# Kernel optimization log

Measured on AMD Instinct MI355X. Metric: run time of the kernel, lower is better.

The kernel has to match this reference:

```python
import jax, jax.numpy as jnp
import numpy as np

ALPHA = 0.2  # leaky relu negative slope (LinearNet default)


def _init_linear(key, fan_in, fan_out):
    kw, kb = jax.random.split(key)
    lim = 1.0 / np.sqrt(fan_in)
    W = jax.random.uniform(kw, (fan_in, fan_out), jnp.float32, -lim, lim)
    b = jax.random.uniform(kb, (fan_out,), jnp.float32, -lim, lim)
    return W, b


def setup_inputs() -> dict:
    key = jax.random.key(0)
    keys = jax.random.split(key, 8)
    B, N, F = 8, 512, 32
    x = jax.random.normal(keys[0], (B, N, F), jnp.float32)
    # fe: [2F=64 -> 64 -> 64 -> 64], all layers leaky-relu (final_linear=False)
    fe_W0, fe_b0 = _init_linear(keys[1], 2 * F, 64)
    fe_W1, fe_b1 = _init_linear(keys[2], 64, 64)
    fe_W2, fe_b2 = _init_linear(keys[3], 64, 64)
    # fn: [64 + F = 96 -> 128 -> 128 -> 32], last layer linear (final_linear=True)
    fn_W0, fn_b0 = _init_linear(keys[4], 64 + F, 128)
    fn_W1, fn_b1 = _init_linear(keys[5], 128, 128)
    fn_W2, fn_b2 = _init_linear(keys[6], 128, 32)
    return {
        "x": x,
        "fe_W0": fe_W0, "fe_b0": fe_b0,
        "fe_W1": fe_W1, "fe_b1": fe_b1,
        "fe_W2": fe_W2, "fe_b2": fe_b2,
        "fn_W0": fn_W0, "fn_b0": fn_b0,
        "fn_W1": fn_W1, "fn_b1": fn_b1,
        "fn_W2": fn_W2, "fn_b2": fn_b2,
    }


def reference(x, fe_W0, fe_b0, fe_W1, fe_b1, fe_W2, fe_b2,
              fn_W0, fn_b0, fn_W1, fn_b1, fn_W2, fn_b2):
    B, N, F = x.shape
    # all-pairs edge inputs: A[b,i,j] = concat(x[b,i], x[b,j])  (x1=repeat rows, x2=tile)
    xi = jnp.broadcast_to(x[:, :, None, :], (B, N, N, F))
    xj = jnp.broadcast_to(x[:, None, :, :], (B, N, N, F))
    A = jnp.concatenate([xi, xj], axis=-1)  # [B, N, N, 2F]
    # edge MLP fe: leaky relu after every layer (final_linear=False)
    for W, b in ((fe_W0, fe_b0), (fe_W1, fe_b1), (fe_W2, fe_b2)):
        A = jax.nn.leaky_relu(A @ W + b, negative_slope=ALPHA)
    # sum aggregation over the sender axis j
    agg = jnp.sum(A, axis=2)  # [B, N, K]
    h = jnp.concatenate([agg, x], axis=-1)  # [B, N, K + F]
    # node MLP fn: leaky relu on hidden layers, final layer linear
    h = jax.nn.leaky_relu(h @ fn_W0 + fn_b0, negative_slope=ALPHA)
    h = jax.nn.leaky_relu(h @ fn_W1 + fn_b1, negative_slope=ALPHA)
    out = h @ fn_W2 + fn_b2  # [B, N, output_node_size]
    return out
```

## Files before the change

kernel.cpp:

```cpp
#include <hip/hip_runtime.h>
#include <hip/hip_bf16.h>

#define ALPHA 0.2f
static __device__ __forceinline__ float lrel(float x) { return fmaxf(x, ALPHA * x); }

typedef __attribute__((ext_vector_type(8))) short bf16x8;
typedef __attribute__((ext_vector_type(4))) float f32x4;

union FragU { bf16x8 v; unsigned int u[4]; uint4 q; };

static __device__ __forceinline__ unsigned int pk2(float a, float b) {
    unsigned int r;
    asm("v_cvt_pk_bf16_f32 %0, %1, %2" : "=v"(r) : "v"(a), "v"(b));
    return r;
}
static __device__ __forceinline__ unsigned int cvl2(float a, float b) {
    return pk2(lrel(a), lrel(b));
}
static __device__ __forceinline__ unsigned short f2bf(float x) {
    union { float f; unsigned int u; } c;
    c.f = x;
    unsigned int r = c.u + 0x7FFFu + ((c.u >> 16) & 1u);
    return (unsigned short)(r >> 16);
}
static __device__ __forceinline__ int pi64(int s) {
    return 32 * ((s >> 4) >> 1) + 8 * ((s >> 2) & 3) + 4 * ((s >> 4) & 1) + (s & 3);
}

__global__ __launch_bounds__(256) void k_uv(
    const float* __restrict__ x, const float* __restrict__ W0, const float* __restrict__ b0,
    const float* __restrict__ W1, const float* __restrict__ W2,
    float* __restrict__ Upi, unsigned short* __restrict__ xbf, unsigned int* __restrict__ WF)
{
    if (blockIdx.x == 1024) {
        const int t = threadIdx.x;
        const int l = t & 63, part = t >> 6;
        const int lo = l & 15, g = l >> 4;
        for (int ff = part; ff < 20; ff += 4) {
            unsigned int o[4];
            if (ff < 4) {
                const int nf = ff;
                const int pc = 32 * (nf >> 1) + 8 * (lo >> 2) + 4 * (nf & 1) + (lo & 3);
#pragma unroll
                for (int uq = 0; uq < 4; ++uq) {
                    const int k0 = 8 * g + 2 * uq;
                    o[uq] = pk2(W0[(32 + k0) * 64 + pc], W0[(33 + k0) * 64 + pc]);
                }
            } else if (ff < 12) {
                const int s = (ff - 4) >> 2, nf = (ff - 4) & 3;
                const int pc = 32 * (nf >> 1) + 8 * (lo >> 2) + 4 * (nf & 1) + (lo & 3);
#pragma unroll
                for (int uq = 0; uq < 4; ++uq) {
                    const int k0 = 32 * s + 8 * g + 2 * uq;
                    o[uq] = pk2(W1[k0 * 64 + pc], W1[(k0 + 1) * 64 + pc]);
                }
            } else {
                const int s = (ff - 12) >> 2, nf = (ff - 12) & 3;
                const int c2 = 16 * nf + lo;
#pragma unroll
                for (int uq = 0; uq < 4; ++uq) {
                    const int k0 = 32 * s + 8 * g + 2 * uq;
                    o[uq] = pk2(W2[k0 * 64 + c2], W2[(k0 + 1) * 64 + c2]);
                }
            }
            *(uint4*)(WF + (ff * 64 + l) * 4) = make_uint4(o[0], o[1], o[2], o[3]);
        }
        return;
    }
    const int idx = blockIdx.x * 256 + threadIdx.x;
    const int n = idx >> 6;
    const int slot = idx & 63;
    const int f = pi64(slot);
    const float* xr = x + n * 32;
    float u = b0[f];
#pragma unroll
    for (int i = 0; i < 32; ++i) u += xr[i] * W0[i * 64 + f];
    Upi[idx] = u;
    if (slot < 32) xbf[n * 32 + slot] = f2bf(xr[slot]);
}

__global__ __launch_bounds__(256, 3) void k_edge(
    const float* __restrict__ Upi, const unsigned short* __restrict__ xbf,
    const unsigned int* __restrict__ WF,
    const float* __restrict__ b1, const float* __restrict__ b2,
    float* __restrict__ AGG)
{
    __shared__ uint4 wlds[1024];
    const int tid = threadIdx.x;
    const int w = tid >> 6, l = tid & 63;
    const int lo = l & 15, g = l >> 4;
    const int bid = blockIdx.x;
    const int b = bid >> 7, ig = bid & 127;
    const int node = b * 512 + ig * 4 + w;

    for (int idx = tid; idx < 1024; idx += 256)
        wlds[idx] = ((const uint4*)WF)[256 + idx];

    FragU w0f[4];
    const uint4* wp = (const uint4*)WF;
#pragma unroll
    for (int nf = 0; nf < 4; ++nf) w0f[nf].q = wp[nf * 64 + l];

    f32x4 u0f[4], b1f[4], b2f[4];
#pragma unroll
    for (int nf = 0; nf < 4; ++nf) {
        const float4 t0 = *(const float4*)(Upi + node * 64 + nf * 16 + 4 * g);
        u0f[nf] = (f32x4){t0.x, t0.y, t0.z, t0.w};
        const float4 t1 = *(const float4*)(b1 + 32 * (nf >> 1) + 8 * g + 4 * (nf & 1));
        const float4 t2 = *(const float4*)(b2 + 16 * nf + 4 * g);
        b1f[nf] = (f32x4){t1.x, t1.y, t1.z, t1.w};
        b2f[nf] = (f32x4){t2.x, t2.y, t2.z, t2.w};
    }

    const unsigned short* xb = xbf + b * 512 * 32;
    FragU xj;
    xj.q = *(const uint4*)(xb + lo * 32 + 8 * g);

    f32x4 agg[4];
#pragma unroll
    for (int nf = 0; nf < 4; ++nf) { f32x4 z = {0.f, 0.f, 0.f, 0.f}; agg[nf] = z; }

    __syncthreads();

#pragma unroll 1
    for (int k = 0; k < 32; ++k) {
        int widx = 0;
        asm volatile("" : "+v"(widx));

        const int jn = ((k + 1) & 31) * 16;
        FragU xjn;
        xjn.q = *(const uint4*)(xb + (jn + lo) * 32 + 8 * g);

        f32x4 acc0[4];
#pragma unroll
        for (int nf = 0; nf < 4; ++nf)
            acc0[nf] = __builtin_amdgcn_mfma_f32_16x16x32_bf16(w0f[nf].v, xj.v, u0f[nf], 0, 0, 0);

        FragU q0, q1;
        q0.u[0] = cvl2(acc0[0][0], acc0[0][1]);
        q0.u[1] = cvl2(acc0[0][2], acc0[0][3]);
        q0.u[2] = cvl2(acc0[1][0], acc0[1][1]);
        q0.u[3] = cvl2(acc0[1][2], acc0[1][3]);
        q1.u[0] = cvl2(acc0[2][0], acc0[2][1]);
        q1.u[1] = cvl2(acc0[2][2], acc0[2][3]);
        q1.u[2] = cvl2(acc0[3][0], acc0[3][1]);
        q1.u[3] = cvl2(acc0[3][2], acc0[3][3]);

        f32x4 acc1[4];
#pragma unroll
        for (int nf = 0; nf < 4; ++nf) {
            FragU wa, wb;
            wa.q = wlds[widx + nf * 64 + l];
            wb.q = wlds[widx + (4 + nf) * 64 + l];
            acc1[nf] = __builtin_amdgcn_mfma_f32_16x16x32_bf16(wa.v, q0.v, b1f[nf], 0, 0, 0);
            acc1[nf] = __builtin_amdgcn_mfma_f32_16x16x32_bf16(wb.v, q1.v, acc1[nf], 0, 0, 0);
        }

        FragU p0, p1;
        p0.u[0] = cvl2(acc1[0][0], acc1[0][1]);
        p0.u[1] = cvl2(acc1[0][2], acc1[0][3]);
        p0.u[2] = cvl2(acc1[1][0], acc1[1][1]);
        p0.u[3] = cvl2(acc1[1][2], acc1[1][3]);
        p1.u[0] = cvl2(acc1[2][0], acc1[2][1]);
        p1.u[1] = cvl2(acc1[2][2], acc1[2][3]);
        p1.u[2] = cvl2(acc1[3][0], acc1[3][1]);
        p1.u[3] = cvl2(acc1[3][2], acc1[3][3]);

        f32x4 acc2[4];
#pragma unroll
        for (int nf = 0; nf < 4; ++nf) {
            FragU wa, wb;
            wa.q = wlds[widx + (8 + nf) * 64 + l];
            wb.q = wlds[widx + (12 + nf) * 64 + l];
            acc2[nf] = __builtin_amdgcn_mfma_f32_16x16x32_bf16(wa.v, p0.v, b2f[nf], 0, 0, 0);
            acc2[nf] = __builtin_amdgcn_mfma_f32_16x16x32_bf16(wb.v, p1.v, acc2[nf], 0, 0, 0);
        }

#pragma unroll
        for (int nf = 0; nf < 4; ++nf)
#pragma unroll
            for (int r = 0; r < 4; ++r) agg[nf][r] += lrel(acc2[nf][r]);

        xj = xjn;
    }

#pragma unroll
    for (int nf = 0; nf < 4; ++nf)
#pragma unroll
        for (int r = 0; r < 4; ++r) {
            float v = agg[nf][r];
            v += __shfl_xor(v, 1);
            v += __shfl_xor(v, 2);
            v += __shfl_xor(v, 4);
            v += __shfl_xor(v, 8);
            agg[nf][r] = v;
        }
    if (lo == 0) {
#pragma unroll
        for (int nf = 0; nf < 4; ++nf) {
            float4 o = {agg[nf][0], agg[nf][1], agg[nf][2], agg[nf][3]};
            *(float4*)(AGG + node * 64 + 16 * nf + 4 * g) = o;
        }
    }
}

__global__ __launch_bounds__(256) void k_fn(
    const float* __restrict__ AGG, const float* __restrict__ x,
    const float* __restrict__ W0, const float* __restrict__ b0,
    const float* __restrict__ W1, const float* __restrict__ b1,
    const float* __restrict__ W2, const float* __restrict__ b2,
    float* __restrict__ out)
{
    __shared__ float in96T[96][8];
    __shared__ float h1T[128][8];
    __shared__ float h2T[128][8];
    const int t = threadIdx.x;
    const int half = t >> 7, f = t & 127;
    const int node0 = blockIdx.x * 8;

    for (int idx = t; idx < 768; idx += 256) {
        int nn = idx & 7, k = idx >> 3;
        in96T[k][nn] = (k < 64) ? AGG[(node0 + nn) * 64 + k]
                                : x[(node0 + nn) * 32 + (k - 64)];
    }
    __syncthreads();

    {
        float a0 = b0[f], a1 = a0, a2 = a0, a3 = a0;
#pragma unroll 4
        for (int k = 0; k < 96; ++k) {
            const float4 iv = *(const float4*)(&in96T[k][4 * half]);
            const float wv = W0[k * 128 + f];
            a0 += iv.x * wv; a1 += iv.y * wv; a2 += iv.z * wv; a3 += iv.w * wv;
        }
        float4 o = {lrel(a0), lrel(a1), lrel(a2), lrel(a3)};
        *(float4*)(&h1T[f][4 * half]) = o;
    }
    __syncthreads();

    {
        float a0 = b1[f], a1 = a0, a2 = a0, a3 = a0;
#pragma unroll 4
        for (int k = 0; k < 128; ++k) {
            const float4 iv = *(const float4*)(&h1T[k][4 * half]);
            const float wv = W1[k * 128 + f];
            a0 += iv.x * wv; a1 += iv.y * wv; a2 += iv.z * wv; a3 += iv.w * wv;
        }
        float4 o = {lrel(a0), lrel(a1), lrel(a2), lrel(a3)};
        *(float4*)(&h2T[f][4 * half]) = o;
    }
    __syncthreads();

    {
        const int nn = t >> 5, fo = t & 31;
        float a = b2[fo];
#pragma unroll 4
        for (int k = 0; k < 128; ++k) a += h2T[k][nn] * W2[k * 32 + fo];
        out[(node0 + nn) * 32 + fo] = a;
    }
}

extern "C" void kernel_launch(void* const* d_in, const int* in_sizes, int n_in,
                              void* d_out, int out_size, void* d_ws, size_t ws_size,
                              hipStream_t stream)
{
    const float* x    = (const float*)d_in[0];
    const float* feW0 = (const float*)d_in[1];
    const float* feb0 = (const float*)d_in[2];
    const float* feW1 = (const float*)d_in[3];
    const float* feb1 = (const float*)d_in[4];
    const float* feW2 = (const float*)d_in[5];
    const float* feb2 = (const float*)d_in[6];
    const float* fnW0 = (const float*)d_in[7];
    const float* fnb0 = (const float*)d_in[8];
    const float* fnW1 = (const float*)d_in[9];
    const float* fnb1 = (const float*)d_in[10];
    const float* fnW2 = (const float*)d_in[11];
    const float* fnb2 = (const float*)d_in[12];
    float* out = (float*)d_out;

    float* Upi = (float*)d_ws;
    float* AGG = Upi + 262144;
    unsigned short* xbf = (unsigned short*)(AGG + 262144);
    unsigned int* WF = (unsigned int*)(xbf + 131072);

    hipLaunchKernelGGL(k_uv,   dim3(1025), dim3(256), 0, stream, x, feW0, feb0, feW1, feW2, Upi, xbf, WF);
    hipLaunchKernelGGL(k_edge, dim3(1024), dim3(256), 0, stream, Upi, xbf, WF, feb1, feb2, AGG);
    hipLaunchKernelGGL(k_fn,   dim3(512),  dim3(256), 0, stream, AGG, x, fnW0, fnb0, fnW1, fnb1, fnW2, fnb2, out);
}
```

Measured before the change: 83.14 us.

## Software-pipeline edge MLP layers across iterations and split leaky-relu sum algebraically

The edge loop is software-pipelined. Layer-0 MFMAs for the next j-tile are issued while the current tile goes through layer 1, and the layer-2 output is accumulated one iteration late, overlapping MFMA latency with VALU conversion work. The leaky-relu-then-sum is rewritten as 0.6*sum(x)+0.4*sum(|x|), using a VALU add with the abs source modifier, and x is prefetched two tiles ahead. Occupancy hint drops from 3 to 2 blocks per CU to make room for the extra live registers, at the risk of less latency hiding across waves.

Result: faster. 74.54 us (-10.3%).

```diff
diff --git a/kernel.cpp b/kernel.cpp
--- a/kernel.cpp
+++ b/kernel.cpp
@@ -16,6 +16,9 @@
 }
 static __device__ __forceinline__ unsigned int cvl2(float a, float b) {
     return pk2(lrel(a), lrel(b));
+}
+static __device__ __forceinline__ void addabs(float& a, float x) {
+    asm("v_add_f32 %0, %0, |%1|" : "+v"(a) : "v"(x));
 }
 static __device__ __forceinline__ unsigned short f2bf(float x) {
     union { float f; unsigned int u; } c;
@@ -79,7 +82,7 @@
     if (slot < 32) xbf[n * 32 + slot] = f2bf(xr[slot]);
 }
 
-__global__ __launch_bounds__(256, 3) void k_edge(
+__global__ __launch_bounds__(256, 2) void k_edge(
     const float* __restrict__ Upi, const unsigned short* __restrict__ xbf,
     const unsigned int* __restrict__ WF,
     const float* __restrict__ b1, const float* __restrict__ b2,
@@ -113,38 +116,52 @@
     }
 
     const unsigned short* xb = xbf + b * 512 * 32;
-    FragU xj;
-    xj.q = *(const uint4*)(xb + lo * 32 + 8 * g);
-
-    f32x4 agg[4];
-#pragma unroll
-    for (int nf = 0; nf < 4; ++nf) { f32x4 z = {0.f, 0.f, 0.f, 0.f}; agg[nf] = z; }
+
+    FragU xjB, xjN;
+    xjB.q = *(const uint4*)(xb + lo * 32 + 8 * g);
+    xjN.q = *(const uint4*)(xb + (16 + lo) * 32 + 8 * g);
 
     __syncthreads();
 
-#pragma unroll 1
+    f32x4 acc0c[4];
+#pragma unroll
+    for (int nf = 0; nf < 4; ++nf)
+        acc0c[nf] = __builtin_amdgcn_mfma_f32_16x16x32_bf16(w0f[nf].v, xjB.v, u0f[nf], 0, 0, 0);
+    xjB = xjN;
+
+    f32x4 acc2p[4];
+#pragma unroll
+    for (int nf = 0; nf < 4; ++nf) { f32x4 z = {0.f, 0.f, 0.f, 0.f}; acc2p[nf] = z; }
+
+    float aggL[4][4], aggA[4][4];
+#pragma unroll
+    for (int nf = 0; nf < 4; ++nf)
+#pragma unroll
+        for (int r = 0; r < 4; ++r) { aggL[nf][r] = 0.f; aggA[nf][r] = 0.f; }
+
+#pragma unroll 2
     for (int k = 0; k < 32; ++k) {
         int widx = 0;
         asm volatile("" : "+v"(widx));
 
-        const int jn = ((k + 1) & 31) * 16;
+        const int jn = ((k + 2) & 31) * 16;
         FragU xjn;
         xjn.q = *(const uint4*)(xb + (jn + lo) * 32 + 8 * g);
 
-        f32x4 acc0[4];
+        f32x4 acc0n[4];
 #pragma unroll
         for (int nf = 0; nf < 4; ++nf)
-            acc0[nf] = __builtin_amdgcn_mfma_f32_16x16x32_bf16(w0f[nf].v, xj.v, u0f[nf], 0, 0, 0);
+            acc0n[nf] = __builtin_amdgcn_mfma_f32_16x16x32_bf16(w0f[nf].v, xjB.v, u0f[nf], 0, 0, 0);
 
         FragU q0, q1;
-        q0.u[0] = cvl2(acc0[0][0], acc0[0][1]);
-        q0.u[1] = cvl2(acc0[0][2], acc0[0][3]);
-        q0.u[2] = cvl2(acc0[1][0], acc0[1][1]);
-        q0.u[3] = cvl2(acc0[1][2], acc0[1][3]);
-        q1.u[0] = cvl2(acc0[2][0], acc0[2][1]);
-        q1.u[1] = cvl2(acc0[2][2], acc0[2][3]);
-        q1.u[2] = cvl2(acc0[3][0], acc0[3][1]);
-        q1.u[3] = cvl2(acc0[3][2], acc0[3][3]);
+        q0.u[0] = cvl2(acc0c[0][0], acc0c[0][1]);
+        q0.u[1] = cvl2(acc0c[0][2], acc0c[0][3]);
+        q0.u[2] = cvl2(acc0c[1][0], acc0c[1][1]);
+        q0.u[3] = cvl2(acc0c[1][2], acc0c[1][3]);
+        q1.u[0] = cvl2(acc0c[2][0], acc0c[2][1]);
+        q1.u[1] = cvl2(acc0c[2][2], acc0c[2][3]);
+        q1.u[2] = cvl2(acc0c[3][0], acc0c[3][1]);
+        q1.u[3] = cvl2(acc0c[3][2], acc0c[3][3]);
 
         f32x4 acc1[4];
 #pragma unroll
@@ -155,6 +172,14 @@
             acc1[nf] = __builtin_amdgcn_mfma_f32_16x16x32_bf16(wa.v, q0.v, b1f[nf], 0, 0, 0);
             acc1[nf] = __builtin_amdgcn_mfma_f32_16x16x32_bf16(wb.v, q1.v, acc1[nf], 0, 0, 0);
         }
+
+#pragma unroll
+        for (int nf = 0; nf < 4; ++nf)
+#pragma unroll
+            for (int r = 0; r < 4; ++r) {
+                aggL[nf][r] += acc2p[nf][r];
+                addabs(aggA[nf][r], acc2p[nf][r]);
+            }
 
         FragU p0, p1;
         p0.u[0] = cvl2(acc1[0][0], acc1[0][1]);
@@ -166,39 +191,43 @@
         p1.u[2] = cvl2(acc1[3][0], acc1[3][1]);
         p1.u[3] = cvl2(acc1[3][2], acc1[3][3]);
 
-        f32x4 acc2[4];
 #pragma unroll
         for (int nf = 0; nf < 4; ++nf) {
             FragU wa, wb;
             wa.q = wlds[widx + (8 + nf) * 64 + l];
             wb.q = wlds[widx + (12 + nf) * 64 + l];
-            acc2[nf] = __builtin_amdgcn_mfma_f32_16x16x32_bf16(wa.v, p0.v, b2f[nf], 0, 0, 0);
-            acc2[nf] = __builtin_amdgcn_mfma_f32_16x16x32_bf16(wb.v, p1.v, acc2[nf], 0, 0, 0);
-        }
-
-#pragma unroll
-        for (int nf = 0; nf < 4; ++nf)
-#pragma unroll
-            for (int r = 0; r < 4; ++r) agg[nf][r] += lrel(acc2[nf][r]);
-
-        xj = xjn;
+            acc2p[nf] = __builtin_amdgcn_mfma_f32_16x16x32_bf16(wa.v, p0.v, b2f[nf], 0, 0, 0);
+            acc2p[nf] = __builtin_amdgcn_mfma_f32_16x16x32_bf16(wb.v, p1.v, acc2p[nf], 0, 0, 0);
+        }
+
+#pragma unroll
+        for (int nf = 0; nf < 4; ++nf) acc0c[nf] = acc0n[nf];
+        xjB = xjn;
     }
 
 #pragma unroll
     for (int nf = 0; nf < 4; ++nf)
 #pragma unroll
         for (int r = 0; r < 4; ++r) {
-            float v = agg[nf][r];
+            aggL[nf][r] += acc2p[nf][r];
+            addabs(aggA[nf][r], acc2p[nf][r]);
+        }
+
+#pragma unroll
+    for (int nf = 0; nf < 4; ++nf)
+#pragma unroll
+        for (int r = 0; r < 4; ++r) {
+            float v = 0.6f * aggL[nf][r] + 0.4f * aggA[nf][r];
             v += __shfl_xor(v, 1);
             v += __shfl_xor(v, 2);
             v += __shfl_xor(v, 4);
             v += __shfl_xor(v, 8);
-            agg[nf][r] = v;
+            aggL[nf][r] = v;
         }
     if (lo == 0) {
 #pragma unroll
         for (int nf = 0; nf < 4; ++nf) {
-            float4 o = {agg[nf][0], agg[nf][1], agg[nf][2], agg[nf][3]};
+            float4 o = {aggL[nf][0], aggL[nf][1], aggL[nf][2], aggL[nf][3]};
             *(float4*)(AGG + node * 64 + 16 * nf + 4 * g) = o;
         }
     }
```

## Process two receiver nodes per wave in edge kernel to reuse weights

Applied to the files above, without the earlier changes.

Each wave in the edge MLP kernel now handles two receiver nodes instead of one. The two nodes share the x_j fragments and the weight fragments read from LDS, and their independent MFMA chains are interleaved to hide latency. The grid is halved to 512 blocks and the occupancy hint drops from 3 to 2 blocks per SM to make room for the doubled accumulator registers. The trade-off is fewer resident waves, and 512 blocks may not fill all compute units evenly.

Result: faster. 77.31 us (-7.0%).

```diff
diff --git a/kernel.cpp b/kernel.cpp
--- a/kernel.cpp
+++ b/kernel.cpp
@@ -79,7 +79,7 @@
     if (slot < 32) xbf[n * 32 + slot] = f2bf(xr[slot]);
 }
 
-__global__ __launch_bounds__(256, 3) void k_edge(
+__global__ __launch_bounds__(256, 2) void k_edge(
     const float* __restrict__ Upi, const unsigned short* __restrict__ xbf,
     const unsigned int* __restrict__ WF,
     const float* __restrict__ b1, const float* __restrict__ b2,
@@ -90,8 +90,9 @@
     const int w = tid >> 6, l = tid & 63;
     const int lo = l & 15, g = l >> 4;
     const int bid = blockIdx.x;
-    const int b = bid >> 7, ig = bid & 127;
-    const int node = b * 512 + ig * 4 + w;
+    const int b = bid >> 6, ig = bid & 63;
+    const int nodeA = b * 512 + ig * 8 + w;
+    const int nodeB = nodeA + 4;
 
     for (int idx = tid; idx < 1024; idx += 256)
         wlds[idx] = ((const uint4*)WF)[256 + idx];
@@ -101,11 +102,13 @@
 #pragma unroll
     for (int nf = 0; nf < 4; ++nf) w0f[nf].q = wp[nf * 64 + l];
 
-    f32x4 u0f[4], b1f[4], b2f[4];
+    f32x4 uA[4], uB[4], b1f[4], b2f[4];
 #pragma unroll
     for (int nf = 0; nf < 4; ++nf) {
-        const float4 t0 = *(const float4*)(Upi + node * 64 + nf * 16 + 4 * g);
-        u0f[nf] = (f32x4){t0.x, t0.y, t0.z, t0.w};
+        const float4 ta = *(const float4*)(Upi + nodeA * 64 + nf * 16 + 4 * g);
+        const float4 tb = *(const float4*)(Upi + nodeB * 64 + nf * 16 + 4 * g);
+        uA[nf] = (f32x4){ta.x, ta.y, ta.z, ta.w};
+        uB[nf] = (f32x4){tb.x, tb.y, tb.z, tb.w};
         const float4 t1 = *(const float4*)(b1 + 32 * (nf >> 1) + 8 * g + 4 * (nf & 1));
         const float4 t2 = *(const float4*)(b2 + 16 * nf + 4 * g);
         b1f[nf] = (f32x4){t1.x, t1.y, t1.z, t1.w};
@@ -116,9 +119,11 @@
     FragU xj;
     xj.q = *(const uint4*)(xb + lo * 32 + 8 * g);
 
-    f32x4 agg[4];
-#pragma unroll
-    for (int nf = 0; nf < 4; ++nf) { f32x4 z = {0.f, 0.f, 0.f, 0.f}; agg[nf] = z; }
+    float aggA[4][4], aggB[4][4];
+#pragma unroll
+    for (int nf = 0; nf < 4; ++nf)
+#pragma unroll
+        for (int r = 0; r < 4; ++r) { aggA[nf][r] = 0.f; aggB[nf][r] = 0.f; }
 
     __syncthreads();
 
@@ -131,55 +136,101 @@
         FragU xjn;
         xjn.q = *(const uint4*)(xb + (jn + lo) * 32 + 8 * g);
 
-        f32x4 acc0[4];
-#pragma unroll
-        for (int nf = 0; nf < 4; ++nf)
-            acc0[nf] = __builtin_amdgcn_mfma_f32_16x16x32_bf16(w0f[nf].v, xj.v, u0f[nf], 0, 0, 0);
-
-        FragU q0, q1;
-        q0.u[0] = cvl2(acc0[0][0], acc0[0][1]);
-        q0.u[1] = cvl2(acc0[0][2], acc0[0][3]);
-        q0.u[2] = cvl2(acc0[1][0], acc0[1][1]);
-        q0.u[3] = cvl2(acc0[1][2], acc0[1][3]);
-        q1.u[0] = cvl2(acc0[2][0], acc0[2][1]);
-        q1.u[1] = cvl2(acc0[2][2], acc0[2][3]);
-        q1.u[2] = cvl2(acc0[3][0], acc0[3][1]);
-        q1.u[3] = cvl2(acc0[3][2], acc0[3][3]);
-
-        f32x4 acc1[4];
+        f32x4 a0A[4], a0B[4];
+#pragma unroll
+        for (int nf = 0; nf < 4; ++nf) {
+            a0A[nf] = __builtin_amdgcn_mfma_f32_16x16x32_bf16(w0f[nf].v, xj.v, uA[nf], 0, 0, 0);
+            a0B[nf] = __builtin_amdgcn_mfma_f32_16x16x32_bf16(w0f[nf].v, xj.v, uB[nf], 0, 0, 0);
+        }
+
+        FragU qA0, qA1;
+        qA0.u[0] = cvl2(a0A[0][0], a0A[0][1]);
+        qA0.u[1] = cvl2(a0A[0][2], a0A[0][3]);
+        qA0.u[2] = cvl2(a0A[1][0], a0A[1][1]);
+        qA0.u[3] = cvl2(a0A[1][2], a0A[1][3]);
+        qA1.u[0] = cvl2(a0A[2][0], a0A[2][1]);
+        qA1.u[1] = cvl2(a0A[2][2], a0A[2][3]);
+        qA1.u[2] = cvl2(a0A[3][0], a0A[3][1]);
+        qA1.u[3] = cvl2(a0A[3][2], a0A[3][3]);
+
+        f32x4 a1A[4];
 #pragma unroll
         for (int nf = 0; nf < 4; ++nf) {
             FragU wa, wb;
             wa.q = wlds[widx + nf * 64 + l];
             wb.q = wlds[widx + (4 + nf) * 64 + l];
-            acc1[nf] = __builtin_amdgcn_mfma_f32_16x16x32_bf16(wa.v, q0.v, b1f[nf], 0, 0, 0);
-            acc1[nf] = __builtin_amdgcn_mfma_f32_16x16x32_bf16(wb.v, q1.v, acc1[nf], 0, 0, 0);
-        }
-
-        FragU p0, p1;
-        p0.u[0] = cvl2(acc1[0][0], acc1[0][1]);
-        p0.u[1] = cvl2(acc1[0][2], acc1[0][3]);
-        p0.u[2] = cvl2(acc1[1][0], acc1[1][1]);
-        p0.u[3] = cvl2(acc1[1][2], acc1[1][3]);
-        p1.u[0] = cvl2(acc1[2][0], acc1[2][1]);
-        p1.u[1] = cvl2(acc1[2][2], acc1[2][3]);
-        p1.u[2] = cvl2(acc1[3][0], acc1[3][1]);
-        p1.u[3] = cvl2(acc1[3][2], acc1[3][3]);
-
-        f32x4 acc2[4];
+            a1A[nf] = __builtin_amdgcn_mfma_f32_16x16x32_bf16(wa.v, qA0.v, b1f[nf], 0, 0, 0);
+            a1A[nf] = __builtin_amdgcn_mfma_f32_16x16x32_bf16(wb.v, qA1.v, a1A[nf], 0, 0, 0);
+        }
+
+        FragU qB0, qB1;
+        qB0.u[0] = cvl2(a0B[0][0], a0B[0][1]);
+        qB0.u[1] = cvl2(a0B[0][2], a0B[0][3]);
+        qB0.u[2] = cvl2(a0B[1][0], a0B[1][1]);
+        qB0.u[3] = cvl2(a0B[1][2], a0B[1][3]);
+        qB1.u[0] = cvl2(a0B[2][0], a0B[2][1]);
+        qB1.u[1] = cvl2(a0B[2][2], a0B[2][3]);
+        qB1.u[2] = cvl2(a0B[3][0], a0B[3][1]);
+        qB1.u[3] = cvl2(a0B[3][2], a0B[3][3]);
+
+        f32x4 a1B[4];
+#pragma unroll
+        for (int nf = 0; nf < 4; ++nf) {
+            FragU wa, wb;
+            wa.q = wlds[widx + nf * 64 + l];
+            wb.q = wlds[widx + (4 + nf) * 64 + l];
+            a1B[nf] = __builtin_amdgcn_mfma_f32_16x16x32_bf16(wa.v, qB0.v, b1f[nf], 0, 0, 0);
+            a1B[nf] = __builtin_amdgcn_mfma_f32_16x16x32_bf16(wb.v, qB1.v, a1B[nf], 0, 0, 0);
+        }
+
+        FragU pA0, pA1;
+        pA0.u[0] = cvl2(a1A[0][0], a1A[0][1]);
+        pA0.u[1] = cvl2(a1A[0][2], a1A[0][3]);
+        pA0.u[2] = cvl2(a1A[1][0], a1A[1][1]);
+        pA0.u[3] = cvl2(a1A[1][2], a1A[1][3]);
+        pA1.u[0] = cvl2(a1A[2][0], a1A[2][1]);
+        pA1.u[1] = cvl2(a1A[2][2], a1A[2][3]);
+        pA1.u[2] = cvl2(a1A[3][0], a1A[3][1]);
+        pA1.u[3] = cvl2(a1A[3][2], a1A[3][3]);
+
+        f32x4 a2A[4];
 #pragma unroll
         for (int nf = 0; nf < 4; ++nf) {
             FragU wa, wb;
             wa.q = wlds[widx + (8 + nf) * 64 + l];
             wb.q = wlds[widx + (12 + nf) * 64 + l];
-            acc2[nf] = __builtin_amdgcn_mfma_f32_16x16x32_bf16(wa.v, p0.v, b2f[nf], 0, 0, 0);
-            acc2[nf] = __builtin_amdgcn_mfma_f32_16x16x32_bf16(wb.v, p1.v, acc2[nf], 0, 0, 0);
+            a2A[nf] = __builtin_amdgcn_mfma_f32_16x16x32_bf16(wa.v, pA0.v, b2f[nf], 0, 0, 0);
+            a2A[nf] = __builtin_amdgcn_mfma_f32_16x16x32_bf16(wb.v, pA1.v, a2A[nf], 0, 0, 0);
+        }
+
+        FragU pB0, pB1;
+        pB0.u[0] = cvl2(a1B[0][0], a1B[0][1]);
+        pB0.u[1] = cvl2(a1B[0][2], a1B[0][3]);
+        pB0.u[2] = cvl2(a1B[1][0], a1B[1][1]);
+        pB0.u[3] = cvl2(a1B[1][2], a1B[1][3]);
+        pB1.u[0] = cvl2(a1B[2][0], a1B[2][1]);
+        pB1.u[1] = cvl2(a1B[2][2], a1B[2][3]);
+        pB1.u[2] = cvl2(a1B[3][0], a1B[3][1]);
+        pB1.u[3] = cvl2(a1B[3][2], a1B[3][3]);
+
+        f32x4 a2B[4];
+#pragma unroll
+        for (int nf = 0; nf < 4; ++nf) {
+            FragU wa, wb;
+            wa.q = wlds[widx + (8 + nf) * 64 + l];
+            wb.q = wlds[widx + (12 + nf) * 64 + l];
+            a2B[nf] = __builtin_amdgcn_mfma_f32_16x16x32_bf16(wa.v, pB0.v, b2f[nf], 0, 0, 0);
+            a2B[nf] = __builtin_amdgcn_mfma_f32_16x16x32_bf16(wb.v, pB1.v, a2B[nf], 0, 0, 0);
         }
 
 #pragma unroll
         for (int nf = 0; nf < 4; ++nf)
 #pragma unroll
-            for (int r = 0; r < 4; ++r) agg[nf][r] += lrel(acc2[nf][r]);
+            for (int r = 0; r < 4; ++r) aggA[nf][r] += lrel(a2A[nf][r]);
+#pragma unroll
+        for (int nf = 0; nf < 4; ++nf)
+#pragma unroll
+            for (int r = 0; r < 4; ++r) aggB[nf][r] += lrel(a2B[nf][r]);
 
         xj = xjn;
     }
@@ -188,18 +239,26 @@
     for (int nf = 0; nf < 4; ++nf)
 #pragma unroll
         for (int r = 0; r < 4; ++r) {
-            float v = agg[nf][r];
-            v += __shfl_xor(v, 1);
-            v += __shfl_xor(v, 2);
-            v += __shfl_xor(v, 4);
-            v += __shfl_xor(v, 8);
-            agg[nf][r] = v;
+            float va = aggA[nf][r];
+            va += __shfl_xor(va, 1);
+            va += __shfl_xor(va, 2);
+            va += __shfl_xor(va, 4);
+            va += __shfl_xor(va, 8);
+            aggA[nf][r] = va;
+            float vb = aggB[nf][r];
+            vb += __shfl_xor(vb, 1);
+            vb += __shfl_xor(vb, 2);
+            vb += __shfl_xor(vb, 4);
+            vb += __shfl_xor(vb, 8);
+            aggB[nf][r] = vb;
         }
     if (lo == 0) {
 #pragma unroll
         for (int nf = 0; nf < 4; ++nf) {
-            float4 o = {agg[nf][0], agg[nf][1], agg[nf][2], agg[nf][3]};
-            *(float4*)(AGG + node * 64 + 16 * nf + 4 * g) = o;
+            float4 oa = {aggA[nf][0], aggA[nf][1], aggA[nf][2], aggA[nf][3]};
+            *(float4*)(AGG + nodeA * 64 + 16 * nf + 4 * g) = oa;
+            float4 ob = {aggB[nf][0], aggB[nf][1], aggB[nf][2], aggB[nf][3]};
+            *(float4*)(AGG + nodeB * 64 + 16 * nf + 4 * g) = ob;
         }
     }
 }
@@ -285,6 +344,6 @@
     unsigned int* WF = (unsigned int*)(xbf + 131072);
 
     hipLaunchKernelGGL(k_uv,   dim3(1025), dim3(256), 0, stream, x, feW0, feb0, feW1, feW2, Upi, xbf, WF);
-    hipLaunchKernelGGL(k_edge, dim3(1024), dim3(256), 0, stream, Upi, xbf, WF, feb1, feb2, AGG);
+    hipLaunchKernelGGL(k_edge, dim3(512),  dim3(256), 0, stream, Upi, xbf, WF, feb1, feb2, AGG);
     hipLaunchKernelGGL(k_fn,   dim3(512),  dim3(256), 0, stream, AGG, x, fnW0, fnb0, fnW1, fnb1, fnW2, fnb2, out);
 }
```

## Switch edge MLP to 32x32x16 MFMA tiles with remapped weight layout

Applied to the files above, without the earlier changes.

Rewrites the edge kernel to use 32x32x16 bf16 MFMAs instead of 16x16x32. Each wave now processes 32 sender nodes per iteration over 16 iterations, and the weight fragment packing and K-permutation are redone to match the new accumulator layout. The aim is fewer MFMA issues and less per-instruction overhead per edge. It also computes leaky-relu accumulation as fma(0.6,x,0.4|x|) and lowers occupancy to 2 blocks per CU to make room for the larger accumulators, at the cost of more register pressure and less latency hiding.

Measured after the change: 81.23 us. 1.02x faster.

```diff
diff --git a/kernel.cpp b/kernel.cpp
--- a/kernel.cpp
+++ b/kernel.cpp
@@ -5,7 +5,7 @@
 static __device__ __forceinline__ float lrel(float x) { return fmaxf(x, ALPHA * x); }
 
 typedef __attribute__((ext_vector_type(8))) short bf16x8;
-typedef __attribute__((ext_vector_type(4))) float f32x4;
+typedef __attribute__((ext_vector_type(16))) float f32x16;
 
 union FragU { bf16x8 v; unsigned int u[4]; uint4 q; };
 
@@ -23,64 +23,75 @@
     unsigned int r = c.u + 0x7FFFu + ((c.u >> 16) & 1u);
     return (unsigned short)(r >> 16);
 }
-static __device__ __forceinline__ int pi64(int s) {
-    return 32 * ((s >> 4) >> 1) + 8 * ((s >> 2) & 3) + 4 * ((s >> 4) & 1) + (s & 3);
+static __device__ __forceinline__ int kslot(int k) {
+    const int c = k >> 4, lh = (k >> 3) & 1, e = k & 7;
+    const int rh = c >> 1, b = 2 * (c & 1) + ((e >> 2) & 1), a = e & 3;
+    return 32 * rh + 8 * b + 4 * lh + a;
 }
 
 __global__ __launch_bounds__(256) void k_uv(
     const float* __restrict__ x, const float* __restrict__ W0, const float* __restrict__ b0,
     const float* __restrict__ W1, const float* __restrict__ W2,
-    float* __restrict__ Upi, unsigned short* __restrict__ xbf, unsigned int* __restrict__ WF)
+    float* __restrict__ U, unsigned short* __restrict__ xbf, unsigned int* __restrict__ WF)
 {
     if (blockIdx.x == 1024) {
         const int t = threadIdx.x;
         const int l = t & 63, part = t >> 6;
-        const int lo = l & 15, g = l >> 4;
-        for (int ff = part; ff < 20; ff += 4) {
+        const int lo32 = l & 31, lh = l >> 5;
+        for (int f = part; f < 20; f += 4) {
             unsigned int o[4];
-            if (ff < 4) {
-                const int nf = ff;
-                const int pc = 32 * (nf >> 1) + 8 * (lo >> 2) + 4 * (nf & 1) + (lo & 3);
-#pragma unroll
-                for (int uq = 0; uq < 4; ++uq) {
-                    const int k0 = 8 * g + 2 * uq;
-                    o[uq] = pk2(W0[(32 + k0) * 64 + pc], W0[(33 + k0) * 64 + pc]);
+            if (f < 4) {
+                const int rh = f >> 1, c = f & 1;
+#pragma unroll
+                for (int q = 0; q < 4; ++q) {
+                    const int k0 = 16 * c + 8 * lh + 2 * q;
+                    o[q] = pk2(W0[(32 + k0) * 64 + 32 * rh + lo32],
+                               W0[(33 + k0) * 64 + 32 * rh + lo32]);
                 }
-            } else if (ff < 12) {
-                const int s = (ff - 4) >> 2, nf = (ff - 4) & 3;
-                const int pc = 32 * (nf >> 1) + 8 * (lo >> 2) + 4 * (nf & 1) + (lo & 3);
-#pragma unroll
-                for (int uq = 0; uq < 4; ++uq) {
-                    const int k0 = 32 * s + 8 * g + 2 * uq;
-                    o[uq] = pk2(W1[k0 * 64 + pc], W1[(k0 + 1) * 64 + pc]);
+            } else if (f < 12) {
+                const int idx = f - 4, rh = idx >> 2, c = idx & 3;
+#pragma unroll
+                for (int q = 0; q < 4; ++q) {
+                    const int k0 = 16 * c + 8 * lh + 2 * q;
+                    o[q] = pk2(W1[kslot(k0) * 64 + 32 * rh + lo32],
+                               W1[kslot(k0 + 1) * 64 + 32 * rh + lo32]);
                 }
             } else {
-                const int s = (ff - 12) >> 2, nf = (ff - 12) & 3;
-                const int c2 = 16 * nf + lo;
-#pragma unroll
-                for (int uq = 0; uq < 4; ++uq) {
-                    const int k0 = 32 * s + 8 * g + 2 * uq;
-                    o[uq] = pk2(W2[k0 * 64 + c2], W2[(k0 + 1) * 64 + c2]);
+                const int idx = f - 12, rh = idx >> 2, c = idx & 3;
+#pragma unroll
+                for (int q = 0; q < 4; ++q) {
+                    const int k0 = 16 * c + 8 * lh + 2 * q;
+                    o[q] = pk2(W2[kslot(k0) * 64 + 32 * rh + lo32],
+                               W2[kslot(k0 + 1) * 64 + 32 * rh + lo32]);
                 }
             }
-            *(uint4*)(WF + (ff * 64 + l) * 4) = make_uint4(o[0], o[1], o[2], o[3]);
+            *(uint4*)(WF + (f * 64 + l) * 4) = make_uint4(o[0], o[1], o[2], o[3]);
         }
         return;
     }
     const int idx = blockIdx.x * 256 + threadIdx.x;
     const int n = idx >> 6;
-    const int slot = idx & 63;
-    const int f = pi64(slot);
+    const int kf = idx & 63;
     const float* xr = x + n * 32;
-    float u = b0[f];
-#pragma unroll
-    for (int i = 0; i < 32; ++i) u += xr[i] * W0[i * 64 + f];
-    Upi[idx] = u;
-    if (slot < 32) xbf[n * 32 + slot] = f2bf(xr[slot]);
-}
-
-__global__ __launch_bounds__(256, 3) void k_edge(
-    const float* __restrict__ Upi, const unsigned short* __restrict__ xbf,
+    float u = b0[kf];
+#pragma unroll
+    for (int i = 0; i < 32; ++i) u += xr[i] * W0[i * 64 + kf];
+    U[idx] = u;
+    if (kf < 32) xbf[n * 32 + kf] = f2bf(xr[kf]);
+}
+
+#define LOAD_CINIT(dst, base)                                         \
+    {                                                                 \
+        _Pragma("unroll")                                             \
+        for (int j = 0; j < 4; ++j) {                                 \
+            const float4 t4 = *(const float4*)((base) + 4 * lh + 8 * j); \
+            dst[4 * j + 0] = t4.x; dst[4 * j + 1] = t4.y;             \
+            dst[4 * j + 2] = t4.z; dst[4 * j + 3] = t4.w;             \
+        }                                                             \
+    }
+
+__global__ __launch_bounds__(256, 2) void k_edge(
+    const float* __restrict__ U, const unsigned short* __restrict__ xbf,
     const unsigned int* __restrict__ WF,
     const float* __restrict__ b1, const float* __restrict__ b2,
     float* __restrict__ AGG)
@@ -88,7 +99,7 @@
     __shared__ uint4 wlds[1024];
     const int tid = threadIdx.x;
     const int w = tid >> 6, l = tid & 63;
-    const int lo = l & 15, g = l >> 4;
+    const int lo32 = l & 31, lh = l >> 5;
     const int bid = blockIdx.x;
     const int b = bid >> 7, ig = bid & 127;
     const int node = b * 512 + ig * 4 + w;
@@ -99,107 +110,116 @@
     FragU w0f[4];
     const uint4* wp = (const uint4*)WF;
 #pragma unroll
-    for (int nf = 0; nf < 4; ++nf) w0f[nf].q = wp[nf * 64 + l];
-
-    f32x4 u0f[4], b1f[4], b2f[4];
-#pragma unroll
-    for (int nf = 0; nf < 4; ++nf) {
-        const float4 t0 = *(const float4*)(Upi + node * 64 + nf * 16 + 4 * g);
-        u0f[nf] = (f32x4){t0.x, t0.y, t0.z, t0.w};
-        const float4 t1 = *(const float4*)(b1 + 32 * (nf >> 1) + 8 * g + 4 * (nf & 1));
-        const float4 t2 = *(const float4*)(b2 + 16 * nf + 4 * g);
-        b1f[nf] = (f32x4){t1.x, t1.y, t1.z, t1.w};
-        b2f[nf] = (f32x4){t2.x, t2.y, t2.z, t2.w};
-    }
+    for (int f = 0; f < 4; ++f) w0f[f].q = wp[f * 64 + l];
+
+    f32x16 u0fa, u0fb, b1fa, b1fb, b2fa, b2fb;
+    LOAD_CINIT(u0fa, U + node * 64);
+    LOAD_CINIT(u0fb, U + node * 64 + 32);
+    LOAD_CINIT(b1fa, b1);
+    LOAD_CINIT(b1fb, b1 + 32);
+    LOAD_CINIT(b2fa, b2);
+    LOAD_CINIT(b2fb, b2 + 32);
 
     const unsigned short* xb = xbf + b * 512 * 32;
-    FragU xj;
-    xj.q = *(const uint4*)(xb + lo * 32 + 8 * g);
-
-    f32x4 agg[4];
-#pragma unroll
-    for (int nf = 0; nf < 4; ++nf) { f32x4 z = {0.f, 0.f, 0.f, 0.f}; agg[nf] = z; }
+
+    FragU xj0, xj1;
+    xj0.q = *(const uint4*)(xb + lo32 * 32 + 8 * lh);
+    xj1.q = *(const uint4*)(xb + lo32 * 32 + 16 + 8 * lh);
+
+    float agga[16], aggb[16];
+#pragma unroll
+    for (int r = 0; r < 16; ++r) { agga[r] = 0.f; aggb[r] = 0.f; }
 
     __syncthreads();
 
 #pragma unroll 1
-    for (int k = 0; k < 32; ++k) {
+    for (int k = 0; k < 16; ++k) {
         int widx = 0;
         asm volatile("" : "+v"(widx));
 
-        const int jn = ((k + 1) & 31) * 16;
-        FragU xjn;
-        xjn.q = *(const uint4*)(xb + (jn + lo) * 32 + 8 * g);
-
-        f32x4 acc0[4];
-#pragma unroll
-        for (int nf = 0; nf < 4; ++nf)
-            acc0[nf] = __builtin_amdgcn_mfma_f32_16x16x32_bf16(w0f[nf].v, xj.v, u0f[nf], 0, 0, 0);
-
-        FragU q0, q1;
-        q0.u[0] = cvl2(acc0[0][0], acc0[0][1]);
-        q0.u[1] = cvl2(acc0[0][2], acc0[0][3]);
-        q0.u[2] = cvl2(acc0[1][0], acc0[1][1]);
-        q0.u[3] = cvl2(acc0[1][2], acc0[1][3]);
-        q1.u[0] = cvl2(acc0[2][0], acc0[2][1]);
-        q1.u[1] = cvl2(acc0[2][2], acc0[2][3]);
-        q1.u[2] = cvl2(acc0[3][0], acc0[3][1]);
-        q1.u[3] = cvl2(acc0[3][2], acc0[3][3]);
-
-        f32x4 acc1[4];
-#pragma unroll
-        for (int nf = 0; nf < 4; ++nf) {
-            FragU wa, wb;
-            wa.q = wlds[widx + nf * 64 + l];
-            wb.q = wlds[widx + (4 + nf) * 64 + l];
-            acc1[nf] = __builtin_amdgcn_mfma_f32_16x16x32_bf16(wa.v, q0.v, b1f[nf], 0, 0, 0);
-            acc1[nf] = __builtin_amdgcn_mfma_f32_16x16x32_bf16(wb.v, q1.v, acc1[nf], 0, 0, 0);
-        }
-
-        FragU p0, p1;
-        p0.u[0] = cvl2(acc1[0][0], acc1[0][1]);
-        p0.u[1] = cvl2(acc1[0][2], acc1[0][3]);
-        p0.u[2] = cvl2(acc1[1][0], acc1[1][1]);
-        p0.u[3] = cvl2(acc1[1][2], acc1[1][3]);
-        p1.u[0] = cvl2(acc1[2][0], acc1[2][1]);
-        p1.u[1] = cvl2(acc1[2][2], acc1[2][3]);
-        p1.u[2] = cvl2(acc1[3][0], acc1[3][1]);
-        p1.u[3] = cvl2(acc1[3][2], acc1[3][3]);
-
-        f32x4 acc2[4];
-#pragma unroll
-        for (int nf = 0; nf < 4; ++nf) {
-            FragU wa, wb;
-            wa.q = wlds[widx + (8 + nf) * 64 + l];
-            wb.q = wlds[widx + (12 + nf) * 64 + l];
-            acc2[nf] = __builtin_amdgcn_mfma_f32_16x16x32_bf16(wa.v, p0.v, b2f[nf], 0, 0, 0);
-            acc2[nf] = __builtin_amdgcn_mfma_f32_16x16x32_bf16(wb.v, p1.v, acc2[nf], 0, 0, 0);
-        }
-
-#pragma unroll
-        for (int nf = 0; nf < 4; ++nf)
-#pragma unroll
-            for (int r = 0; r < 4; ++r) agg[nf][r] += lrel(acc2[nf][r]);
-
-        xj = xjn;
-    }
-
-#pragma unroll
-    for (int nf = 0; nf < 4; ++nf)
-#pragma unroll
-        for (int r = 0; r < 4; ++r) {
-            float v = agg[nf][r];
-            v += __shfl_xor(v, 1);
-            v += __shfl_xor(v, 2);
-            v += __shfl_xor(v, 4);
-            v += __shfl_xor(v, 8);
-            agg[nf][r] = v;
-        }
-    if (lo == 0) {
-#pragma unroll
-        for (int nf = 0; nf < 4; ++nf) {
-            float4 o = {agg[nf][0], agg[nf][1], agg[nf][2], agg[nf][3]};
-            *(float4*)(AGG + node * 64 + 16 * nf + 4 * g) = o;
+        const int jn = ((k + 1) & 15) * 32;
+        FragU xjn0, xjn1;
+        xjn0.q = *(const uint4*)(xb + (jn + lo32) * 32 + 8 * lh);
+        xjn1.q = *(const uint4*)(xb + (jn + lo32) * 32 + 16 + 8 * lh);
+
+        f32x16 acc0a = __builtin_amdgcn_mfma_f32_32x32x16_bf16(w0f[0].v, xj0.v, u0fa, 0, 0, 0);
+        f32x16 acc0b = __builtin_amdgcn_mfma_f32_32x32x16_bf16(w0f[2].v, xj0.v, u0fb, 0, 0, 0);
+        acc0a = __builtin_amdgcn_mfma_f32_32x32x16_bf16(w0f[1].v, xj1.v, acc0a, 0, 0, 0);
+        acc0b = __builtin_amdgcn_mfma_f32_32x32x16_bf16(w0f[3].v, xj1.v, acc0b, 0, 0, 0);
+
+        FragU q0, q1, q2, q3;
+        q0.u[0] = cvl2(acc0a[0],  acc0a[1]);  q0.u[1] = cvl2(acc0a[2],  acc0a[3]);
+        q0.u[2] = cvl2(acc0a[4],  acc0a[5]);  q0.u[3] = cvl2(acc0a[6],  acc0a[7]);
+        q1.u[0] = cvl2(acc0a[8],  acc0a[9]);  q1.u[1] = cvl2(acc0a[10], acc0a[11]);
+        q1.u[2] = cvl2(acc0a[12], acc0a[13]); q1.u[3] = cvl2(acc0a[14], acc0a[15]);
+        q2.u[0] = cvl2(acc0b[0],  acc0b[1]);  q2.u[1] = cvl2(acc0b[2],  acc0b[3]);
+        q2.u[2] = cvl2(acc0b[4],  acc0b[5]);  q2.u[3] = cvl2(acc0b[6],  acc0b[7]);
+        q3.u[0] = cvl2(acc0b[8],  acc0b[9]);  q3.u[1] = cvl2(acc0b[10], acc0b[11]);
+        q3.u[2] = cvl2(acc0b[12], acc0b[13]); q3.u[3] = cvl2(acc0b[14], acc0b[15]);
+
+        FragU wa, wb;
+        wa.q = wlds[widx + 0 * 64 + l]; wb.q = wlds[widx + 4 * 64 + l];
+        f32x16 acc1a = __builtin_amdgcn_mfma_f32_32x32x16_bf16(wa.v, q0.v, b1fa, 0, 0, 0);
+        f32x16 acc1b = __builtin_amdgcn_mfma_f32_32x32x16_bf16(wb.v, q0.v, b1fb, 0, 0, 0);
+        wa.q = wlds[widx + 1 * 64 + l]; wb.q = wlds[widx + 5 * 64 + l];
+        acc1a = __builtin_amdgcn_mfma_f32_32x32x16_bf16(wa.v, q1.v, acc1a, 0, 0, 0);
+        acc1b = __builtin_amdgcn_mfma_f32_32x32x16_bf16(wb.v, q1.v, acc1b, 0, 0, 0);
+        wa.q = wlds[widx + 2 * 64 + l]; wb.q = wlds[widx + 6 * 64 + l];
+        acc1a = __builtin_amdgcn_mfma_f32_32x32x16_bf16(wa.v, q2.v, acc1a, 0, 0, 0);
+        acc1b = __builtin_amdgcn_mfma_f32_32x32x16_bf16(wb.v, q2.v, acc1b, 0, 0, 0);
+        wa.q = wlds[widx + 3 * 64 + l]; wb.q = wlds[widx + 7 * 64 + l];
+        acc1a = __builtin_amdgcn_mfma_f32_32x32x16_bf16(wa.v, q3.v, acc1a, 0, 0, 0);
+        acc1b = __builtin_amdgcn_mfma_f32_32x32x16_bf16(wb.v, q3.v, acc1b, 0, 0, 0);
+
+        FragU p0, p1, p2, p3;
+        p0.u[0] = cvl2(acc1a[0],  acc1a[1]);  p0.u[1] = cvl2(acc1a[2],  acc1a[3]);
+        p0.u[2] = cvl2(acc1a[4],  acc1a[5]);  p0.u[3] = cvl2(acc1a[6],  acc1a[7]);
+        p1.u[0] = cvl2(acc1a[8],  acc1a[9]);  p1.u[1] = cvl2(acc1a[10], acc1a[11]);
+        p1.u[2] = cvl2(acc1a[12], acc1a[13]); p1.u[3] = cvl2(acc1a[14], acc1a[15]);
+        p2.u[0] = cvl2(acc1b[0],  acc1b[1]);  p2.u[1] = cvl2(acc1b[2],  acc1b[3]);
+        p2.u[2] = cvl2(acc1b[4],  acc1b[5]);  p2.u[3] = cvl2(acc1b[6],  acc1b[7]);
+        p3.u[0] = cvl2(acc1b[8],  acc1b[9]);  p3.u[1] = cvl2(acc1b[10], acc1b[11]);
+        p3.u[2] = cvl2(acc1b[12], acc1b[13]); p3.u[3] = cvl2(acc1b[14], acc1b[15]);
+
+        wa.q = wlds[widx + 8 * 64 + l];  wb.q = wlds[widx + 12 * 64 + l];
+        f32x16 acc2a = __builtin_amdgcn_mfma_f32_32x32x16_bf16(wa.v, p0.v, b2fa, 0, 0, 0);
+        f32x16 acc2b = __builtin_amdgcn_mfma_f32_32x32x16_bf16(wb.v, p0.v, b2fb, 0, 0, 0);
+        wa.q = wlds[widx + 9 * 64 + l];  wb.q = wlds[widx + 13 * 64 + l];
+        acc2a = __builtin_amdgcn_mfma_f32_32x32x16_bf16(wa.v, p1.v, acc2a, 0, 0, 0);
+        acc2b = __builtin_amdgcn_mfma_f32_32x32x16_bf16(wb.v, p1.v, acc2b, 0, 0, 0);
+        wa.q = wlds[widx + 10 * 64 + l]; wb.q = wlds[widx + 14 * 64 + l];
+        acc2a = __builtin_amdgcn_mfma_f32_32x32x16_bf16(wa.v, p2.v, acc2a, 0, 0, 0);
+        acc2b = __builtin_amdgcn_mfma_f32_32x32x16_bf16(wb.v, p2.v, acc2b, 0, 0, 0);
+        wa.q = wlds[widx + 11 * 64 + l]; wb.q = wlds[widx + 15 * 64 + l];
+        acc2a = __builtin_amdgcn_mfma_f32_32x32x16_bf16(wa.v, p3.v, acc2a, 0, 0, 0);
+        acc2b = __builtin_amdgcn_mfma_f32_32x32x16_bf16(wb.v, p3.v, acc2b, 0, 0, 0);
+
+#pragma unroll
+        for (int r = 0; r < 16; ++r) {
+            agga[r] = fmaf(0.6f, acc2a[r], fmaf(0.4f, fabsf(acc2a[r]), agga[r]));
+            aggb[r] = fmaf(0.6f, acc2b[r], fmaf(0.4f, fabsf(acc2b[r]), aggb[r]));
+        }
+
+        xj0 = xjn0; xj1 = xjn1;
+    }
+
+#pragma unroll
+    for (int r = 0; r < 16; ++r) {
+        float va = agga[r], vb = aggb[r];
+        va += __shfl_xor(va, 1);  vb += __shfl_xor(vb, 1);
+        va += __shfl_xor(va, 2);  vb += __shfl_xor(vb, 2);
+        va += __shfl_xor(va, 4);  vb += __shfl_xor(vb, 4);
+        va += __shfl_xor(va, 8);  vb += __shfl_xor(vb, 8);
+        va += __shfl_xor(va, 16); vb += __shfl_xor(vb, 16);
+        agga[r] = va; aggb[r] = vb;
+    }
+    if (lo32 == 0) {
+#pragma unroll
+        for (int j = 0; j < 4; ++j) {
+            float4 oa = {agga[4 * j], agga[4 * j + 1], agga[4 * j + 2], agga[4 * j + 3]};
+            *(float4*)(AGG + node * 64 + 4 * lh + 8 * j) = oa;
+            float4 ob = {aggb[4 * j], aggb[4 * j + 1], aggb[4 * j + 2], aggb[4 * j + 3]};
+            *(float4*)(AGG + node * 64 + 32 + 4 * lh + 8 * j) = ob;
         }
     }
 }
@@ -279,12 +299,12 @@
     const float* fnb2 = (const float*)d_in[12];
     float* out = (float*)d_out;
 
-    float* Upi = (float*)d_ws;
-    float* AGG = Upi + 262144;
+    float* U   = (float*)d_ws;
+    float* AGG = U + 262144;
     unsigned short* xbf = (unsigned short*)(AGG + 262144);
     unsigned int* WF = (unsigned int*)(xbf + 131072);
 
-    hipLaunchKernelGGL(k_uv,   dim3(1025), dim3(256), 0, stream, x, feW0, feb0, feW1, feW2, Upi, xbf, WF);
-    hipLaunchKernelGGL(k_edge, dim3(1024), dim3(256), 0, stream, Upi, xbf, WF, feb1, feb2, AGG);
+    hipLaunchKernelGGL(k_uv,   dim3(1025), dim3(256), 0, stream, x, feW0, feb0, feW1, feW2, U, xbf, WF);
+    hipLaunchKernelGGL(k_edge, dim3(1024), dim3(256), 0, stream, U, xbf, WF, feb1, feb2, AGG);
     hipLaunchKernelGGL(k_fn,   dim3(512),  dim3(256), 0, stream, AGG, x, fnW0, fnb0, fnW1, fnb1, fnW2, fnb2, out);
 }
```
